# Kernel optimization log

Measured on AMD Instinct MI355X. Metric: run time of the kernel, lower is better.

## Reference

```python
import jax, jax.numpy as jnp
import numpy as np

TEMP = 0.07
NUM_CLASSES = 4

def setup_inputs() -> dict:
    key = jax.random.key(0)
    k1, k2 = jax.random.split(key)
    features_in = jax.random.normal(k1, (4, 64, 2048), dtype=jnp.float32)
    labels_in = jax.random.randint(k2, (4, 2048), 0, NUM_CLASSES, dtype=jnp.int64)
    return {"features_in": features_in, "labels_in": labels_in}

def reference(features_in, labels_in):
    B, C, N = features_in.shape
    M = B * N
    # torch .view(C, B*N): row-major reinterpret of contiguous [B,C,N]
    feats = features_in.reshape(C, M).T            # [M, C]
    labels = labels_in.reshape(-1)                 # [M]

    # per-class keep probability: min(750/(count+1), 1), gathered by label
    counts = jnp.bincount(labels, length=NUM_CLASSES)
    keep_p = jnp.minimum(750.0 / (counts.astype(jnp.float32) + 1.0), 1.0)
    p = keep_p[labels]                             # [M]
    sel = jax.random.bernoulli(jax.random.key(42), p)  # [M] bool, stochastic subsample

    # L2 normalize rows; original divides by norms of already-normalized rows (==1)
    nv = feats / jnp.linalg.norm(feats, axis=1, keepdims=True)
    sim = nv @ nv.T                                # [M, M] cosine similarities
    dp = jnp.exp(sim / TEMP)
    dp = dp * (1.0 - jnp.eye(M, dtype=dp.dtype))   # zero the diagonal

    same = labels[:, None] == labels[None, :]
    pair = sel[:, None] & sel[None, :]             # both points kept
    pos = jnp.sum(jnp.where(same & pair, dp, 0.0), axis=1)
    neg = jnp.sum(jnp.where((~same) & pair, dp, 0.0), axis=1)

    frac = pos / (pos + neg)
    per = -jnp.log(jnp.where(sel, frac, 1.0))      # guard unselected rows
    n_sel = jnp.maximum(jnp.sum(sel), 1)
    loss = jnp.sum(jnp.where(sel, per, 0.0)) / n_sel
    return loss
```

## Files before the change

### kernel.cpp

```cpp
#include <hip/hip_runtime.h>
#include <hip/hip_bf16.h>

#define M_TOT 8192
#define NCLS 4
#define NSEL_CAP 4096
#define NT 64

typedef __attribute__((ext_vector_type(8)))  short short8v;
typedef __attribute__((ext_vector_type(16))) float f32x16;

__device__ __forceinline__ unsigned int rotl32(unsigned int x, unsigned int r) {
    return (x << r) | (x >> (32u - r));
}

__device__ unsigned int threefry_bits_key42(unsigned int m) {
    const unsigned int ks0 = 0u;
    const unsigned int ks1 = 42u;
    const unsigned int ks2 = 0x1BD11BDAu ^ 0u ^ 42u;
    unsigned int j  = (m < 4096u) ? m : (m - 4096u);
    unsigned int x0 = j + ks0;
    unsigned int x1 = (j + 4096u) + ks1;
#define TF_RND(r) { x0 += x1; x1 = rotl32(x1, (r)); x1 ^= x0; }
    TF_RND(13u) TF_RND(15u) TF_RND(26u) TF_RND(6u)
    x0 += ks1; x1 += ks2 + 1u;
    TF_RND(17u) TF_RND(29u) TF_RND(16u) TF_RND(24u)
    x0 += ks2; x1 += ks0 + 2u;
    TF_RND(13u) TF_RND(15u) TF_RND(26u) TF_RND(6u)
    x0 += ks0; x1 += ks1 + 3u;
    TF_RND(17u) TF_RND(29u) TF_RND(16u) TF_RND(24u)
    x0 += ks1; x1 += ks2 + 4u;
    TF_RND(13u) TF_RND(15u) TF_RND(26u) TF_RND(6u)
    x0 += ks2; x1 += ks0 + 5u;
#undef TF_RND
    return (m < 4096u) ? x0 : x1;
}

__device__ __forceinline__ unsigned short f2bf(float x) {
    const unsigned int u = __float_as_uint(x);
    return (unsigned short)((u + 0x7FFFu + ((u >> 16) & 1u)) >> 16);
}
__device__ __forceinline__ float bf2f(unsigned short b) {
    return __uint_as_float(((unsigned int)b) << 16);
}

__global__ void select_kernel(const int* __restrict__ labels,
                              int* __restrict__ nsel_g,
                              int* __restrict__ sel_idx,
                              int* __restrict__ lab_sel) {
    __shared__ int   hist[NCLS];
    __shared__ float keepp[NCLS];
    __shared__ int   wtot[4];
    const int t = threadIdx.x;
    const int lane = t & 63, w = t >> 6;
    if (t < NCLS) hist[t] = 0;
    __syncthreads();

    const int m0 = t * 32;
    int c0 = 0, c1 = 0, c2 = 0, c3 = 0;
    for (int r = 0; r < 32; ++r) {
        const int lab = labels[m0 + r];
        c0 += (lab == 0); c1 += (lab == 1); c2 += (lab == 2); c3 += (lab == 3);
    }
    int cc[4] = {c0, c1, c2, c3};
    #pragma unroll
    for (int cls = 0; cls < NCLS; ++cls) {
        int v = cc[cls];
        for (int off = 32; off > 0; off >>= 1) v += __shfl_down(v, off, 64);
        if (lane == 0) atomicAdd(&hist[cls], v);
    }
    __syncthreads();
    if (t < NCLS) keepp[t] = fminf(750.0f / ((float)hist[t] + 1.0f), 1.0f);
    __syncthreads();

    unsigned int flags = 0u;
    int cnt = 0;
    for (int r = 0; r < 32; ++r) {
        const int m = m0 + r;
        const unsigned int bits = threefry_bits_key42((unsigned int)m);
        const float u = __uint_as_float((bits >> 9) | 0x3F800000u) - 1.0f;
        if (u < keepp[labels[m]]) { flags |= (1u << r); ++cnt; }
    }
    int x = cnt;
    #pragma unroll
    for (int off = 1; off < 64; off <<= 1) {
        const int y = __shfl_up(x, off, 64);
        if (lane >= off) x += y;
    }
    if (lane == 63) wtot[w] = x;
    const int excl = x - cnt;
    __syncthreads();
    int base = excl;
    for (int w2 = 0; w2 < w; ++w2) base += wtot[w2];
    if (t == 0) *nsel_g = wtot[0] + wtot[1] + wtot[2] + wtot[3];
    for (int r = 0; r < 32; ++r) {
        if (flags & (1u << r)) {
            const int m = m0 + r;
            sel_idx[base] = m;
            lab_sel[base] = labels[m];
            ++base;
        }
    }
}

__global__ void norm_kernel(const float* __restrict__ features,
                            const int* __restrict__ sel_idx,
                            const int* __restrict__ nsel_g,
                            unsigned short* __restrict__ nv_hi,
                            unsigned short* __restrict__ nv_lo,
                            float* __restrict__ pos,
                            float* __restrict__ neg) {
    const int tid = blockIdx.x * 256 + threadIdx.x;
    if (tid < M_TOT) { pos[tid] = 0.0f; neg[tid] = 0.0f; }
    const int p  = tid >> 3;
    const int kg = tid & 7;
    const int nsel = *nsel_g;
    const int ofs = (p << 6) + kg * 8;
    if (p >= nsel) {
        const uint4 z = {0, 0, 0, 0};
        *(uint4*)&nv_hi[ofs] = z;
        *(uint4*)&nv_lo[ofs] = z;
        return;
    }
    const int m = sel_idx[p];
    float v[8];
    float ss = 0.0f;
    #pragma unroll
    for (int q = 0; q < 8; ++q) {
        v[q] = features[(kg * 8 + q) * M_TOT + m];
        ss += v[q] * v[q];
    }
    ss += __shfl_xor(ss, 1, 8);
    ss += __shfl_xor(ss, 2, 8);
    ss += __shfl_xor(ss, 4, 8);
    const float rn = rsqrtf(ss);
    unsigned short hs[8], ls[8];
    #pragma unroll
    for (int q = 0; q < 8; ++q) {
        const float x = v[q] * rn;
        const unsigned short h = f2bf(x);
        hs[q] = h;
        ls[q] = f2bf(x - bf2f(h));
    }
    *(uint4*)&nv_hi[ofs] = *(const uint4*)hs;
    *(uint4*)&nv_lo[ofs] = *(const uint4*)ls;
}

#define EXP2_SCALE 20.609929155556605f

__global__ __launch_bounds__(256, 4) void pair_kernel(
        const unsigned short* __restrict__ nv_hi,
        const unsigned short* __restrict__ nv_lo,
        const int* __restrict__ lab_sel,
        const int* __restrict__ nsel_g,
        float* __restrict__ pos,
        float* __restrict__ neg) {
    const int nsel = *nsel_g;
    const int it = blockIdx.y, jt = blockIdx.x;
    const int i0 = it * 64, j0 = jt * 64;
    if (i0 >= nsel || j0 >= nsel) return;

    __shared__ __align__(16) unsigned short frags[2][2][8][64][8];
    __shared__ int La[64], Lb[64];

    const int t = threadIdx.x;
    const int wave = t >> 6, lane = t & 63;

    #pragma unroll
    for (int it8 = 0; it8 < 8; ++it8) {
        const int slot = it8 * 256 + t;
        const int side  = slot >> 10;
        const int plane = (slot >> 9) & 1;
        const int c     = (slot >> 6) & 7;
        const int row   = slot & 63;
        const unsigned short* src = plane ? nv_lo : nv_hi;
        const int basep = (side ? j0 : i0) + row;
        const uint4 v = *(const uint4*)&src[(basep << 6) + c * 8];
        *(uint4*)&((unsigned short*)frags)[slot * 8] = v;
    }
    if (t < 64)       La[t]      = lab_sel[i0 + t];
    else if (t < 128) Lb[t - 64] = lab_sel[j0 + t - 64];
    __syncthreads();

    const int qi = (wave >> 1) * 32, qj = (wave & 1) * 32;
    const int half = lane >> 5, l31 = lane & 31;
    const int ra = qi + l31, rb = qj + l31;

    f32x16 acc;
    #pragma unroll
    for (int r = 0; r < 16; ++r) acc[r] = 0.0f;

    #pragma unroll
    for (int s = 0; s < 4; ++s) {
        const int c = 2 * s + half;
        const short8v ah = *(const short8v*)&frags[0][0][c][ra][0];
        const short8v al = *(const short8v*)&frags[0][1][c][ra][0];
        const short8v bh = *(const short8v*)&frags[1][0][c][rb][0];
        const short8v bl = *(const short8v*)&frags[1][1][c][rb][0];
        acc = __builtin_amdgcn_mfma_f32_32x32x16_bf16(ah, bh, acc, 0, 0, 0);
        acc = __builtin_amdgcn_mfma_f32_32x32x16_bf16(ah, bl, acc, 0, 0, 0);
        acc = __builtin_amdgcn_mfma_f32_32x32x16_bf16(al, bh, acc, 0, 0, 0);
    }

    const int colL = qj + l31;
    const int jg = j0 + colL;
    const int Lj = Lb[colL];
    float cp = 0.0f, cn = 0.0f;
    #pragma unroll
    for (int r = 0; r < 16; ++r) {
        const int rowL = qi + (r & 3) + 8 * (r >> 2) + 4 * half;
        const int ig = i0 + rowL;
        const bool valid = (ig < nsel) && (jg < nsel) && (ig != jg);
        const float d = valid ? exp2f(acc[r] * EXP2_SCALE) : 0.0f;
        if (La[rowL] == Lj) cp += d; else cn += d;
    }
    cp += __shfl_xor(cp, 32, 64);
    cn += __shfl_xor(cn, 32, 64);
    if (half == 0 && jg < nsel) {
        atomicAdd(&pos[jg], cp);
        atomicAdd(&neg[jg], cn);
    }
}

__global__ void loss_kernel(const float* __restrict__ pos,
                            const float* __restrict__ neg,
                            const int* __restrict__ nsel_g,
                            float* __restrict__ out) {
    const int nsel = *nsel_g;
    float s = 0.0f;
    for (int i = threadIdx.x; i < nsel; i += 256) {
        const float fr = pos[i] / (pos[i] + neg[i]);
        s += -logf(fr);
    }
    __shared__ float red[256];
    red[threadIdx.x] = s;
    __syncthreads();
    for (int off = 128; off > 0; off >>= 1) {
        if (threadIdx.x < off) red[threadIdx.x] += red[threadIdx.x + off];
        __syncthreads();
    }
    if (threadIdx.x == 0) out[0] = red[0] / (float)(nsel > 0 ? nsel : 1);
}

extern "C" void kernel_launch(void* const* d_in, const int* in_sizes, int n_in,
                              void* d_out, int out_size, void* d_ws, size_t ws_size,
                              hipStream_t stream) {
    const float* features = (const float*)d_in[0];
    const int*   labels   = (const int*)d_in[1];
    float*       out      = (float*)d_out;
    char*        ws       = (char*)d_ws;

    int*   nsel_g   = (int*)(ws);
    int*   sel_idx  = (int*)(ws + 1024);
    int*   lab_sel  = (int*)(ws + 1024 + 16384);
    float* pos      = (float*)(ws + 1024 + 32768);
    float* neg      = pos + M_TOT;
    unsigned short* nv_hi = (unsigned short*)(ws + 1024 + 32768 + 65536);
    unsigned short* nv_lo = nv_hi + NSEL_CAP * 64;

    select_kernel<<<1, 256, 0, stream>>>(labels, nsel_g, sel_idx, lab_sel);
    norm_kernel<<<128, 256, 0, stream>>>(features, sel_idx, nsel_g, nv_hi, nv_lo, pos, neg);
    pair_kernel<<<dim3(NT, NT), 256, 0, stream>>>(nv_hi, nv_lo, lab_sel, nsel_g, pos, neg);
    loss_kernel<<<1, 256, 0, stream>>>(pos, neg, nsel_g, out);
}
```

Before: 93.88 us.

## Fuse selection and normalization into one redundant-selection kernel

The single-block selection kernel and the normalization kernel are merged into one 128-block kernel. Each block recomputes the class histogram and Bernoulli mask, compacts the selected indices into LDS, and then normalizes its own slice of 32 points. The Threefry hash now produces both output words per call, so the 8192 draws need half as many hash evaluations. This removes a launch and the global round trip for the index list, at the cost of every block repeating the selection work. Padding rows beyond nsel are no longer zeroed, which relies on pair_kernel masking them.

```diff
diff --git a/kernel.cpp b/kernel.cpp
--- a/kernel.cpp
+++ b/kernel.cpp
@@ -13,11 +13,10 @@
     return (x << r) | (x >> (32u - r));
 }
 
-__device__ unsigned int threefry_bits_key42(unsigned int m) {
+__device__ __forceinline__ uint2 threefry_pair_key42(unsigned int j) {
     const unsigned int ks0 = 0u;
     const unsigned int ks1 = 42u;
     const unsigned int ks2 = 0x1BD11BDAu ^ 0u ^ 42u;
-    unsigned int j  = (m < 4096u) ? m : (m - 4096u);
     unsigned int x0 = j + ks0;
     unsigned int x1 = (j + 4096u) + ks1;
 #define TF_RND(r) { x0 += x1; x1 = rotl32(x1, (r)); x1 ^= x0; }
@@ -32,7 +31,11 @@
     TF_RND(13u) TF_RND(15u) TF_RND(26u) TF_RND(6u)
     x0 += ks2; x1 += ks0 + 5u;
 #undef TF_RND
-    return (m < 4096u) ? x0 : x1;
+    return make_uint2(x0, x1);
+}
+
+__device__ __forceinline__ float bits_to_unit(unsigned int bits) {
+    return __uint_as_float((bits >> 9) | 0x3F800000u) - 1.0f;
 }
 
 __device__ __forceinline__ unsigned short f2bf(float x) {
@@ -43,42 +46,53 @@
     return __uint_as_float(((unsigned int)b) << 16);
 }
 
-__global__ void select_kernel(const int* __restrict__ labels,
-                              int* __restrict__ nsel_g,
-                              int* __restrict__ sel_idx,
-                              int* __restrict__ lab_sel) {
+__global__ __launch_bounds__(256) void select_norm_kernel(
+        const float* __restrict__ features,
+        const int* __restrict__ labels,
+        int* __restrict__ nsel_g,
+        int* __restrict__ lab_sel,
+        unsigned short* __restrict__ nv_hi,
+        unsigned short* __restrict__ nv_lo,
+        float* __restrict__ pos,
+        float* __restrict__ neg) {
     __shared__ int   hist[NCLS];
     __shared__ float keepp[NCLS];
     __shared__ int   wtot[4];
-    const int t = threadIdx.x;
+    __shared__ int   lds_m[NSEL_CAP];
+    const int t = threadIdx.x, b = blockIdx.x;
     const int lane = t & 63, w = t >> 6;
+
+    const int gid = b * 256 + t;
+    if (gid < NSEL_CAP) { pos[gid] = 0.0f; neg[gid] = 0.0f; }
     if (t < NCLS) hist[t] = 0;
     __syncthreads();
 
-    const int m0 = t * 32;
-    int c0 = 0, c1 = 0, c2 = 0, c3 = 0;
-    for (int r = 0; r < 32; ++r) {
-        const int lab = labels[m0 + r];
-        c0 += (lab == 0); c1 += (lab == 1); c2 += (lab == 2); c3 += (lab == 3);
-    }
-    int cc[4] = {c0, c1, c2, c3};
-    #pragma unroll
-    for (int cls = 0; cls < NCLS; ++cls) {
-        int v = cc[cls];
-        for (int off = 32; off > 0; off >>= 1) v += __shfl_down(v, off, 64);
-        if (lane == 0) atomicAdd(&hist[cls], v);
+    {
+        const int m0 = t * 32;
+        int c0 = 0, c1 = 0, c2 = 0, c3 = 0;
+        for (int r = 0; r < 32; ++r) {
+            const int lab = labels[m0 + r];
+            c0 += (lab == 0); c1 += (lab == 1); c2 += (lab == 2); c3 += (lab == 3);
+        }
+        int cc[4] = {c0, c1, c2, c3};
+        #pragma unroll
+        for (int cls = 0; cls < NCLS; ++cls) {
+            int v = cc[cls];
+            for (int off = 32; off > 0; off >>= 1) v += __shfl_down(v, off, 64);
+            if (lane == 0) atomicAdd(&hist[cls], v);
+        }
     }
     __syncthreads();
     if (t < NCLS) keepp[t] = fminf(750.0f / ((float)hist[t] + 1.0f), 1.0f);
     __syncthreads();
 
+    const int jb = t * 16;
     unsigned int flags = 0u;
     int cnt = 0;
-    for (int r = 0; r < 32; ++r) {
-        const int m = m0 + r;
-        const unsigned int bits = threefry_bits_key42((unsigned int)m);
-        const float u = __uint_as_float((bits >> 9) | 0x3F800000u) - 1.0f;
-        if (u < keepp[labels[m]]) { flags |= (1u << r); ++cnt; }
+    for (int r = 0; r < 16; ++r) {
+        const uint2 bb = threefry_pair_key42((unsigned int)(jb + r));
+        if (bits_to_unit(bb.x) < keepp[labels[jb + r]])        { flags |= 1u << r;        ++cnt; }
+        if (bits_to_unit(bb.y) < keepp[labels[jb + r + 4096]]) { flags |= 1u << (16 + r); ++cnt; }
     }
     int x = cnt;
     #pragma unroll
@@ -91,37 +105,19 @@
     __syncthreads();
     int base = excl;
     for (int w2 = 0; w2 < w; ++w2) base += wtot[w2];
-    if (t == 0) *nsel_g = wtot[0] + wtot[1] + wtot[2] + wtot[3];
-    for (int r = 0; r < 32; ++r) {
-        if (flags & (1u << r)) {
-            const int m = m0 + r;
-            sel_idx[base] = m;
-            lab_sel[base] = labels[m];
-            ++base;
-        }
-    }
-}
-
-__global__ void norm_kernel(const float* __restrict__ features,
-                            const int* __restrict__ sel_idx,
-                            const int* __restrict__ nsel_g,
-                            unsigned short* __restrict__ nv_hi,
-                            unsigned short* __restrict__ nv_lo,
-                            float* __restrict__ pos,
-                            float* __restrict__ neg) {
-    const int tid = blockIdx.x * 256 + threadIdx.x;
-    if (tid < M_TOT) { pos[tid] = 0.0f; neg[tid] = 0.0f; }
-    const int p  = tid >> 3;
-    const int kg = tid & 7;
-    const int nsel = *nsel_g;
-    const int ofs = (p << 6) + kg * 8;
-    if (p >= nsel) {
-        const uint4 z = {0, 0, 0, 0};
-        *(uint4*)&nv_hi[ofs] = z;
-        *(uint4*)&nv_lo[ofs] = z;
-        return;
-    }
-    const int m = sel_idx[p];
+    const int nsel = wtot[0] + wtot[1] + wtot[2] + wtot[3];
+    if (b == 0 && t == 0) *nsel_g = nsel;
+    for (int r = 0; r < 16; ++r) {
+        if (flags & (1u << r))        lds_m[base++] = jb + r;
+        if (flags & (1u << (16 + r))) lds_m[base++] = jb + r + 4096;
+    }
+    __syncthreads();
+
+    const int p  = b * 32 + (t >> 3);
+    const int kg = t & 7;
+    if (p >= nsel) return;
+    const int m = lds_m[p];
+    if (kg == 0) lab_sel[p] = labels[m];
     float v[8];
     float ss = 0.0f;
     #pragma unroll
@@ -136,11 +132,12 @@
     unsigned short hs[8], ls[8];
     #pragma unroll
     for (int q = 0; q < 8; ++q) {
-        const float x = v[q] * rn;
-        const unsigned short h = f2bf(x);
+        const float xx = v[q] * rn;
+        const unsigned short h = f2bf(xx);
         hs[q] = h;
-        ls[q] = f2bf(x - bf2f(h));
-    }
+        ls[q] = f2bf(xx - bf2f(h));
+    }
+    const int ofs = (p << 6) + kg * 8;
     *(uint4*)&nv_hi[ofs] = *(const uint4*)hs;
     *(uint4*)&nv_lo[ofs] = *(const uint4*)ls;
 }
@@ -250,15 +247,14 @@
     char*        ws       = (char*)d_ws;
 
     int*   nsel_g   = (int*)(ws);
-    int*   sel_idx  = (int*)(ws + 1024);
-    int*   lab_sel  = (int*)(ws + 1024 + 16384);
-    float* pos      = (float*)(ws + 1024 + 32768);
-    float* neg      = pos + M_TOT;
-    unsigned short* nv_hi = (unsigned short*)(ws + 1024 + 32768 + 65536);
+    int*   lab_sel  = (int*)(ws + 1024);
+    float* pos      = (float*)(ws + 1024 + 16384);
+    float* neg      = pos + NSEL_CAP;
+    unsigned short* nv_hi = (unsigned short*)(ws + 1024 + 16384 + 32768);
     unsigned short* nv_lo = nv_hi + NSEL_CAP * 64;
 
-    select_kernel<<<1, 256, 0, stream>>>(labels, nsel_g, sel_idx, lab_sel);
-    norm_kernel<<<128, 256, 0, stream>>>(features, sel_idx, nsel_g, nv_hi, nv_lo, pos, neg);
+    select_norm_kernel<<<128, 256, 0, stream>>>(features, labels, nsel_g, lab_sel,
+                                                nv_hi, nv_lo, pos, neg);
     pair_kernel<<<dim3(NT, NT), 256, 0, stream>>>(nv_hi, nv_lo, lab_sel, nsel_g, pos, neg);
     loss_kernel<<<1, 256, 0, stream>>>(pos, neg, nsel_g, out);
 }
```

New measurement: 87.73 us. -6.6%, faster.
